# Kernel optimization log

Hardware: AMD Instinct MI355X
Metric: run time of the kernel (lower is better)

The kernel has to match this reference:

```python
import jax, jax.numpy as jnp
import numpy as np

WINDOW = (16, 16)
STRIDE = (8, 8)
PADDING = (0, 0)  # (pad_h, pad_w), applied symmetrically like torch _pair semantics


def setup_inputs() -> dict:
    key = jax.random.key(0)
    x = jax.random.normal(key, (16, 3, 512, 512), dtype=jnp.float32)
    return {"x": x}


def reference(x) -> jnp.ndarray:
    wh, ww = WINDOW
    sh, sw = STRIDE
    ph, pw = PADDING
    if ph or pw:
        x = jnp.pad(x, ((0, 0), (0, 0), (ph, ph), (pw, pw)))
    B, C, H, W = x.shape
    nH = (H - wh) // sh + 1
    nW = (W - ww) // sw + 1
    # overlapping window gather indices
    rows = (jnp.arange(nH) * sh)[:, None] + jnp.arange(wh)[None, :]  # (nH, wh)
    cols = (jnp.arange(nW) * sw)[:, None] + jnp.arange(ww)[None, :]  # (nW, ww)
    # gather: (B, C, nH, nW, wh, ww)
    p = x[:, :, rows[:, None, :, None], cols[None, :, None, :]]
    # permute to (B, nH, nW, C, wh, ww) then flatten patch grid -> (B, N, C, wh, ww)
    p = jnp.transpose(p, (0, 2, 3, 1, 4, 5))
    return p.reshape(B, nH * nW, C, wh, ww)
```

## Files before the change

kernel.cpp:

```cpp
#include <hip/hip_runtime.h>


#define BB 16
#define CC 3
#define HH 512
#define WW 512
#define NH 63
#define NW 63
#define NP (NH * NW)
#define G 3
#define NG (NH / G)
#define ROWS (8 * G + 8)
#define TPB 512

typedef float f4 __attribute__((ext_vector_type(4)));

__device__ __forceinline__ unsigned swz(unsigned row, unsigned col4) {
  return col4 ^ ((row & 3u) << 1);
}

__global__ __launch_bounds__(TPB) void extract_patches_v4(
    const float* __restrict__ x, float* __restrict__ out) {
  __shared__ f4 lds[ROWS * 128];

  unsigned blk = blockIdx.x;
  unsigned id = (blk & 7u) * (BB * CC * NG / 8u) + (blk >> 3);

  unsigned plane = id / NG;
  unsigned g = id - plane * NG;
  unsigned b = plane / CC;
  unsigned c = plane - b * CC;
  unsigned tid = threadIdx.x;

  const f4* src = reinterpret_cast<const f4*>(x) +
                  (((size_t)plane << 9) + 24u * g) * 128u;
  #pragma unroll
  for (int k = 0; k < 8; ++k) {
    unsigned idx = tid + (unsigned)k * TPB;
    unsigned row = idx >> 7;
    unsigned col4 = idx & 127u;
    lds[row * 128u + swz(row, col4)] = src[idx];
  }
  __syncthreads();

  f4* o = reinterpret_cast<f4*>(out);
  size_t obase = ((size_t)b * NP + (size_t)(3u * g) * NW) * (CC * 64u) +
                 (size_t)c * 64u;
  for (unsigned e = tid; e < 3u * NW * 64u; e += TPB) {
    unsigned r = e & 63u;
    unsigned pq = e >> 6;
    unsigned h = pq / NW;
    unsigned pw = pq - h * NW;
    unsigned i = r >> 2;
    unsigned j4 = r & 3u;
    unsigned lrow = 8u * h + i;
    f4 v = lds[lrow * 128u + swz(lrow, 2u * pw + j4)];
    o[obase + (size_t)pq * (CC * 64u) + r] = v;
  }
}

extern "C" void kernel_launch(void* const* d_in, const int* in_sizes, int n_in,
                              void* d_out, int out_size, void* d_ws, size_t ws_size,
                              hipStream_t stream) {
  const float* x = (const float*)d_in[0];
  float* out = (float*)d_out;
  extract_patches_v4<<<dim3(BB * CC * NG), TPB, 0, stream>>>(x, out);
}
```

Baseline: 231.3 us.

## Tile by patch-row and half-width across all channels for contiguous output writes

Each block now covers one patch row and half of the patch columns, loading all three channels' 16-row strips into LDS instead of one channel's 32-row band. Output writes become one fully contiguous span per block rather than strided 64-float4 chunks per channel. The cost is rereading input rows, since neighbouring patch rows overlap by 8 rows and the halves share two columns. LDS reads drop the swizzle and use a padded 66-wide stride, with index arithmetic that uses division.

```diff
diff --git a/kernel.cpp b/kernel.cpp
--- a/kernel.cpp
+++ b/kernel.cpp
@@ -3,59 +3,54 @@
 
 #define BB 16
 #define CC 3
-#define HH 512
-#define WW 512
 #define NH 63
 #define NW 63
 #define NP (NH * NW)
-#define G 3
-#define NG (NH / G)
-#define ROWS (8 * G + 8)
 #define TPB 512
 
 typedef float f4 __attribute__((ext_vector_type(4)));
 
-__device__ __forceinline__ unsigned swz(unsigned row, unsigned col4) {
-  return col4 ^ ((row & 3u) << 1);
-}
-
-__global__ __launch_bounds__(TPB) void extract_patches_v4(
+__global__ __launch_bounds__(TPB) void extract_patches_v5(
     const float* __restrict__ x, float* __restrict__ out) {
-  __shared__ f4 lds[ROWS * 128];
+  __shared__ f4 lds[CC * 16 * 66];
 
   unsigned blk = blockIdx.x;
-  unsigned id = (blk & 7u) * (BB * CC * NG / 8u) + (blk >> 3);
+  unsigned id = (blk & 7u) * 252u + (blk >> 3);
 
-  unsigned plane = id / NG;
-  unsigned g = id - plane * NG;
-  unsigned b = plane / CC;
-  unsigned c = plane - b * CC;
+  unsigned half = id & 1u;
+  unsigned w = id >> 1;
+  unsigned ph = w % NH;
+  unsigned b = w / NH;
   unsigned tid = threadIdx.x;
 
-  const f4* src = reinterpret_cast<const f4*>(x) +
-                  (((size_t)plane << 9) + 24u * g) * 128u;
-  #pragma unroll
-  for (int k = 0; k < 8; ++k) {
-    unsigned idx = tid + (unsigned)k * TPB;
-    unsigned row = idx >> 7;
-    unsigned col4 = idx & 127u;
-    lds[row * 128u + swz(row, col4)] = src[idx];
+  unsigned pw0 = half ? 32u : 0u;
+  unsigned c0  = half ? 64u : 0u;
+  unsigned ncv = half ? 64u : 66u;
+  unsigned npw = half ? 31u : 32u;
+
+  const f4* src = reinterpret_cast<const f4*>(x);
+  unsigned srow = 8u * ph;
+  for (unsigned s = tid; s < CC * 16u * 66u; s += TPB) {
+    unsigned c = s / 1056u;
+    unsigned rem = s - c * 1056u;
+    unsigned row = rem / 66u;
+    unsigned col = rem - row * 66u;
+    if (col < ncv)
+      lds[s] = src[(b * CC + c) * 65536u + (srow + row) * 128u + c0 + col];
   }
   __syncthreads();
 
-  f4* o = reinterpret_cast<f4*>(out);
-  size_t obase = ((size_t)b * NP + (size_t)(3u * g) * NW) * (CC * 64u) +
-                 (size_t)c * 64u;
-  for (unsigned e = tid; e < 3u * NW * 64u; e += TPB) {
+  f4* o = reinterpret_cast<f4*>(out) +
+          ((size_t)b * NP + (size_t)ph * NW + pw0) * (CC * 64u);
+  unsigned ecnt = npw * (CC * 64u);
+  for (unsigned e = tid; e < ecnt; e += TPB) {
+    unsigned q = e >> 6;
     unsigned r = e & 63u;
-    unsigned pq = e >> 6;
-    unsigned h = pq / NW;
-    unsigned pw = pq - h * NW;
+    unsigned pwL = q / 3u;
+    unsigned c = q - pwL * 3u;
     unsigned i = r >> 2;
     unsigned j4 = r & 3u;
-    unsigned lrow = 8u * h + i;
-    f4 v = lds[lrow * 128u + swz(lrow, 2u * pw + j4)];
-    o[obase + (size_t)pq * (CC * 64u) + r] = v;
+    o[e] = lds[c * 1056u + i * 66u + 2u * pwL + j4];
   }
 }
 
@@ -64,5 +59,5 @@
                               hipStream_t stream) {
   const float* x = (const float*)d_in[0];
   float* out = (float*)d_out;
-  extract_patches_v4<<<dim3(BB * CC * NG), TPB, 0, stream>>>(x, out);
+  extract_patches_v5<<<dim3(BB * NH * 2), TPB, 0, stream>>>(x, out);
 }
```

Result: no change. 228.0 us (-1.4%).
